# Kernel tuning notes

Measured on AMD Instinct MI355X. Metric: run time of the kernel, lower is better.

Reference implementation:

```python
import jax, jax.numpy as jnp
import numpy as np

D = 1024  # feature_size

def setup_inputs() -> dict:
    key = jax.random.key(0)
    ks = jax.random.split(key, 9)
    s = 1.0 / np.sqrt(D)
    inp = {"x": jax.random.normal(ks[0], (4, 2048, D), dtype=jnp.float32)}
    names = ["Wk", "Wq", "Wv", "Wo"]
    for i, n in enumerate(names):
        inp[n] = jax.random.uniform(ks[1 + 2 * i], (D, D), dtype=jnp.float32, minval=-s, maxval=s)
        inp["b" + n[1]] = jax.random.uniform(ks[2 + 2 * i], (D,), dtype=jnp.float32, minval=-s, maxval=s)
    return inp

def reference(x, Wk, bk, Wq, bq, Wv, bv, Wo, bo):
    # Linear layers: x @ W.T + b (torch nn.Linear convention)
    keys = jnp.einsum('bsd,ed->bse', x, Wk) + bk
    queries = jnp.einsum('bsd,ed->bse', x, Wq) + bq
    values = jnp.einsum('bsd,ed->bse', x, Wv) + bv
    scale = 1.0 / jnp.sqrt(jnp.float32(D))
    scores = jnp.einsum('bqd,bkd->bqk', queries, keys) * scale  # [B,S,S]
    attention = jax.nn.softmax(scores, axis=-1)
    out = jnp.einsum('bqk,bkd->bqd', attention, values)
    out = jnp.einsum('bsd,ed->bse', out, Wo) + bo
    return (out, attention)
```

## Files before the change

### kernel.cpp

```cpp
#include <hip/hip_runtime.h>
#include <hip/hip_bf16.h>


typedef __attribute__((ext_vector_type(8))) _Float16 f16x8;
typedef __attribute__((ext_vector_type(4))) _Float16 f16x4;
typedef __attribute__((ext_vector_type(4))) float f32x4;

static __device__ __forceinline__ void gl_lds16(const void* g, void* s) {
  __builtin_amdgcn_global_load_lds(
      (const __attribute__((address_space(1))) void*)g,
      (__attribute__((address_space(3))) void*)s, 16, 0, 0);
}

__global__ __launch_bounds__(256) void prep(
    const float* __restrict__ x,
    const float* __restrict__ Wq, const float* __restrict__ Wk,
    const float* __restrict__ Wo, const float* __restrict__ Wv,
    const float* __restrict__ bv, const float* __restrict__ bo,
    _Float16* __restrict__ xh, _Float16* __restrict__ Woh,
    _Float16* __restrict__ WvT, _Float16* __restrict__ WqT,
    _Float16* __restrict__ WkT, float* __restrict__ cpb) {
  const int b = blockIdx.x;
  const int tid = threadIdx.x;
  if (b < 8192) {
    const int i = b * 256 + tid;
    float4 v = reinterpret_cast<const float4*>(x)[i];
    f16x4 r = {(_Float16)v.x, (_Float16)v.y, (_Float16)v.z, (_Float16)v.w};
    reinterpret_cast<f16x4*>(xh)[i] = r;
  } else if (b < 9216) {
    const int i = (b - 8192) * 256 + tid;
    float4 v = reinterpret_cast<const float4*>(Wo)[i];
    f16x4 r = {(_Float16)v.x, (_Float16)v.y, (_Float16)v.z, (_Float16)v.w};
    reinterpret_cast<f16x4*>(Woh)[i] = r;
  } else if (b < 9984) {
    const int bb = b - 9216;
    const int which = bb >> 8;
    const float* src = which == 0 ? Wv : which == 1 ? Wq : Wk;
    _Float16* dst = which == 0 ? WvT : which == 1 ? WqT : WkT;
    __shared__ float t[64][65];
    const int tb = bb & 255;
    const int bx = (tb & 15) * 64, by = (tb >> 4) * 64;
    const int tx = tid & 63, ty = tid >> 6;
#pragma unroll
    for (int i = 0; i < 64; i += 4)
      t[ty + i][tx] = src[(long)(by + ty + i) * 1024 + bx + tx];
    __syncthreads();
#pragma unroll
    for (int i = 0; i < 64; i += 4)
      dst[(long)(bx + ty + i) * 1024 + by + tx] = (_Float16)t[tx][ty + i];
  } else {
    const int n = b - 9984;
    float s = 0.f;
    for (int d = tid; d < 1024; d += 256) s += Wo[(long)n * 1024 + d] * bv[d];
#pragma unroll
    for (int o = 32; o >= 1; o >>= 1) s += __shfl_xor(s, o);
    __shared__ float red[4];
    if ((tid & 63) == 0) red[tid >> 6] = s;
    __syncthreads();
    if (tid == 0) cpb[n] = red[0] + red[1] + red[2] + red[3] + bo[n];
  }
}

__global__ __launch_bounds__(256) void wkern(
    const float* __restrict__ bq, const float* __restrict__ bk,
    const _Float16* __restrict__ WkT, const _Float16* __restrict__ WqT,
    float* __restrict__ w1, float* __restrict__ w2, float* __restrict__ c0) {
  const int b = blockIdx.x;
  const int tid = threadIdx.x;
  float s = 0.f;
  if (b < 1024) {
    for (int e = tid; e < 1024; e += 256) s += bq[e] * (float)WkT[(long)b * 1024 + e];
  } else if (b < 2048) {
    const int d = b - 1024;
    for (int e = tid; e < 1024; e += 256) s += bk[e] * (float)WqT[(long)d * 1024 + e];
  } else {
    for (int e = tid; e < 1024; e += 256) s += bq[e] * bk[e];
  }
#pragma unroll
  for (int o = 32; o >= 1; o >>= 1) s += __shfl_xor(s, o);
  __shared__ float red[4];
  if ((tid & 63) == 0) red[tid >> 6] = s;
  __syncthreads();
  if (tid == 0) {
    const float v = red[0] + red[1] + red[2] + red[3];
    if (b < 1024) w1[b] = v;
    else if (b < 2048) w2[b - 1024] = v;
    else c0[0] = v;
  }
}

__global__ __launch_bounds__(256) void rowcol(
    const _Float16* __restrict__ xh, const float* __restrict__ w1,
    const float* __restrict__ w2, const float* __restrict__ c0,
    float* __restrict__ rowb, float* __restrict__ colb) {
  const long i = blockIdx.x;
  const int tid = threadIdx.x;
  f16x4 xv = reinterpret_cast<const f16x4*>(xh + i * 1024)[tid];
  float4 a1 = reinterpret_cast<const float4*>(w1)[tid];
  float4 a2 = reinterpret_cast<const float4*>(w2)[tid];
  float x0 = (float)xv[0], x1 = (float)xv[1], x2 = (float)xv[2], x3 = (float)xv[3];
  float d1 = x0 * a1.x + x1 * a1.y + x2 * a1.z + x3 * a1.w;
  float d2 = x0 * a2.x + x1 * a2.y + x2 * a2.z + x3 * a2.w;
#pragma unroll
  for (int o = 32; o >= 1; o >>= 1) { d1 += __shfl_xor(d1, o); d2 += __shfl_xor(d2, o); }
  __shared__ float r1[4], r2[4];
  if ((tid & 63) == 0) { r1[tid >> 6] = d1; r2[tid >> 6] = d2; }
  __syncthreads();
  if (tid == 0) {
    colb[i] = (r1[0] + r1[1] + r1[2] + r1[3]) * 0.03125f;
    rowb[i] = (r2[0] + r2[1] + r2[2] + r2[3] + c0[0]) * 0.03125f;
  }
}

template <int EPI, bool BB>
__global__ __launch_bounds__(256) void gemm128(
    const _Float16* __restrict__ A, const _Float16* __restrict__ B,
    const float* __restrict__ bias, float* __restrict__ Cf,
    _Float16* __restrict__ Ch, _Float16* __restrict__ C3,
    int M, int N, int K, long sA, long sB, long sC, float alpha, int panelW) {
  __shared__ _Float16 lds[3][2][4096];

  const unsigned gx = gridDim.x, gy = gridDim.y;
  const unsigned nwg = gx * gy * gridDim.z;
  unsigned flat = (blockIdx.z * gy + blockIdx.y) * gx + blockIdx.x;
  flat = (flat & 7) * (nwg >> 3) + (flat >> 3);
  const unsigned pb = gy * panelW;
  const long bz = flat / (gx * gy);
  const unsigned rem = flat % (gx * gy);
  const unsigned pi = rem / pb;
  const unsigned rem2 = rem % pb;
  const unsigned byi = rem2 / panelW;
  const unsigned bxi = pi * panelW + rem2 % panelW;

  const int tid = threadIdx.x;
  const int w = tid >> 6, lane = tid & 63;
  const int wr = w >> 1, wc = w & 1;
  const int lr = lane & 15, q = lane >> 4;
  const long row0 = (long)byi * 128;
  const long col0 = (long)bxi * 128;
  const int nt = K >> 5;

  const _Float16* pA = A + bz * sA;
  const _Float16* pB = BB ? (B + (row0 >> 11) * sB) : (B + bz * sB);

  f32x4 acc[4][4] = {};

  const int r0 = tid >> 2, c0i = ((tid & 3) - (r0 >> 1)) & 3;
  const int s1 = tid + 256;
  const int r1 = s1 >> 2, c1 = ((s1 & 3) - (r1 >> 1)) & 3;

  auto stage = [&](int kt) {
    if (kt >= nt) return;
    const int bf = kt % 3;
    const long gk = (long)kt * 32;
#pragma unroll
    for (int ab = 0; ab < 2; ++ab) {
      const _Float16* src = ab ? pB : pA;
      const long base = ab ? col0 : row0;
      gl_lds16(src + (base + r0) * (long)K + gk + c0i * 8, &lds[bf][ab][w << 9]);
      gl_lds16(src + (base + r1) * (long)K + gk + c1 * 8, &lds[bf][ab][2048 + (w << 9)]);
    }
  };
  auto rd = [&](int bf, int ab, int r) -> f16x8 {
    const int slot = (r << 2) + ((q + (r >> 1)) & 3);
    return *(const f16x8*)&lds[bf][ab][slot << 3];
  };

  stage(0); stage(1);
  asm volatile("s_waitcnt vmcnt(4)" ::: "memory");
  __builtin_amdgcn_s_barrier();
  __builtin_amdgcn_sched_barrier(0);

  for (int kt = 0; kt < nt; ++kt) {
    const int bf = kt % 3;
    stage(kt + 2);
    f16x8 a[4], b[4];
#pragma unroll
    for (int m = 0; m < 4; ++m) a[m] = rd(bf, 0, wr * 64 + m * 16 + lr);
#pragma unroll
    for (int n = 0; n < 4; ++n) b[n] = rd(bf, 1, wc * 64 + n * 16 + lr);
#pragma unroll
    for (int m = 0; m < 4; ++m)
#pragma unroll
      for (int n = 0; n < 4; ++n)
        acc[m][n] = __builtin_amdgcn_mfma_f32_16x16x32_f16(a[m], b[n], acc[m][n], 0, 0, 0);
    if (kt < nt - 2) asm volatile("s_waitcnt vmcnt(4)" ::: "memory");
    else             asm volatile("s_waitcnt vmcnt(0)" ::: "memory");
    __builtin_amdgcn_s_barrier();
    __builtin_amdgcn_sched_barrier(0);
  }

  if (EPI == 3 && col0 >= 1024) {
    _Float16* t = (_Float16*)&lds[0][0][0];
#pragma unroll
    for (int m = 0; m < 4; ++m)
#pragma unroll
      for (int n = 0; n < 4; ++n)
#pragma unroll
        for (int r = 0; r < 4; ++r) {
          const int rr = wr * 64 + m * 16 + q * 4 + r;
          const int cc = wc * 64 + n * 16 + lr;
          t[cc * 132 + rr] = (_Float16)(acc[m][n][r] * alpha);
        }
    __syncthreads();
    const long b2 = row0 >> 11;
    const long s2b = row0 & 2047;
    const int n = tid >> 1, s0 = (tid & 1) * 64;
    _Float16* dst = C3 + (b2 * 1024 + (col0 - 1024) + n) * 2048 + s2b + s0;
    const _Float16* srcT = t + n * 132 + s0;
#pragma unroll
    for (int j = 0; j < 8; ++j)
      *(f16x8*)(dst + j * 8) = *(const f16x8*)(srcT + j * 8);
    return;
  }

#pragma unroll
  for (int m = 0; m < 4; ++m)
#pragma unroll
    for (int n = 0; n < 4; ++n)
#pragma unroll
      for (int r = 0; r < 4; ++r) {
        const long row = row0 + wr * 64 + m * 16 + q * 4 + r;
        const long col = col0 + wc * 64 + n * 16 + lr;
        float v = acc[m][n][r] * alpha;
        if (EPI == 2) {
          v += Cf[bz * 2048 + row] + bias[bz * 2048 + col];
          Ch[bz * sC + row * (long)N + col] = (_Float16)v;
        } else if (EPI == 0) {
          if (bias) v += bias[col];
          Cf[bz * sC + row * (long)N + col] = v;
        } else if (EPI == 1) {
          if (bias) v += bias[col];
          Ch[bz * sC + row * (long)N + col] = (_Float16)v;
        } else {
          Ch[row * 1024 + col] = (_Float16)v;
        }
      }
}

__global__ __launch_bounds__(256) void softmax16(
    _Float16* __restrict__ Ph, float* __restrict__ attn) {
  const long row = blockIdx.x;
  _Float16* ph = Ph + row * 2048;
  float* ap = attn + row * 2048;
  const int tid = threadIdx.x;
  f16x8 v = reinterpret_cast<const f16x8*>(ph)[tid];
  float x[8];
#pragma unroll
  for (int j = 0; j < 8; ++j) x[j] = (float)v[j];
  float m = x[0];
#pragma unroll
  for (int j = 1; j < 8; ++j) m = fmaxf(m, x[j]);
#pragma unroll
  for (int o = 32; o >= 1; o >>= 1) m = fmaxf(m, __shfl_xor(m, o));
  __shared__ float red[4], red2[4];
  if ((tid & 63) == 0) red[tid >> 6] = m;
  __syncthreads();
  m = fmaxf(fmaxf(red[0], red[1]), fmaxf(red[2], red[3]));
  float s = 0.f;
#pragma unroll
  for (int j = 0; j < 8; ++j) { x[j] = expf(x[j] - m); s += x[j]; }
#pragma unroll
  for (int o = 32; o >= 1; o >>= 1) s += __shfl_xor(s, o);
  if ((tid & 63) == 0) red2[tid >> 6] = s;
  __syncthreads();
  s = red2[0] + red2[1] + red2[2] + red2[3];
  const float inv = 1.0f / s;
#pragma unroll
  for (int j = 0; j < 8; ++j) x[j] *= inv;
  reinterpret_cast<float4*>(ap)[tid * 2] = make_float4(x[0], x[1], x[2], x[3]);
  reinterpret_cast<float4*>(ap)[tid * 2 + 1] = make_float4(x[4], x[5], x[6], x[7]);
  f16x8 pv;
#pragma unroll
  for (int j = 0; j < 8; ++j) pv[j] = (_Float16)x[j];
  reinterpret_cast<f16x8*>(ph)[tid] = pv;
}

extern "C" void kernel_launch(void* const* d_in, const int* in_sizes, int n_in,
                              void* d_out, int out_size, void* d_ws, size_t ws_size,
                              hipStream_t stream) {
  const float* x  = (const float*)d_in[0];
  const float* Wk = (const float*)d_in[1];
  const float* bk = (const float*)d_in[2];
  const float* Wq = (const float*)d_in[3];
  const float* bq = (const float*)d_in[4];
  const float* Wv = (const float*)d_in[5];
  const float* bv = (const float*)d_in[6];
  const float* Wo = (const float*)d_in[7];
  const float* bo = (const float*)d_in[8];

  float* out  = (float*)d_out;
  float* attn = (float*)d_out + 8388608;

  const size_t MB = 1024 * 1024;
  unsigned char* ws = (unsigned char*)d_ws;
  _Float16* xh   = (_Float16*)(ws + 0 * MB);
  _Float16* Wf   = (_Float16*)(ws + 16 * MB);
  _Float16* WqT  = (_Float16*)(ws + 20 * MB);
  _Float16* Woh  = (_Float16*)(ws + 22 * MB);
  _Float16* WvT  = (_Float16*)(ws + 24 * MB);
  _Float16* WkT  = (_Float16*)(ws + 26 * MB);
  float*    rowb = (float*)   (ws + 28 * MB);
  float*    colb = (float*)   (ws + 28 * MB + 32768);
  float*    cpb  = (float*)   (ws + 28 * MB + 65536);
  float*    w1   = (float*)   (ws + 28 * MB + 69632);
  float*    w2   = (float*)   (ws + 28 * MB + 73728);
  float*    c0s  = (float*)   (ws + 28 * MB + 77824);
  _Float16* Y    = (_Float16*)(ws + 29 * MB);
  _Float16* Vt   = (_Float16*)(ws + 45 * MB);
  _Float16* Ph   = (_Float16*)(ws + 61 * MB);

  dim3 blk(256);
  const _Float16* nullh = nullptr;

  hipLaunchKernelGGL(prep, dim3(11008), blk, 0, stream,
                     x, Wq, Wk, Wo, Wv, bv, bo, xh, Woh, WvT, WqT, WkT, cpb);
  hipLaunchKernelGGL(wkern, dim3(2049), blk, 0, stream, bq, bk, WkT, WqT, w1, w2, c0s);
  hipLaunchKernelGGL((gemm128<1, false>), dim3(8, 8, 1), blk, 0, stream,
                     WkT, WqT, (const float*)nullptr, (float*)nullptr,
                     Wf, (_Float16*)nullh,
                     1024, 1024, 1024, 0L, 0L, 0L, 1.0f, 8);
  hipLaunchKernelGGL((gemm128<1, false>), dim3(8, 8, 1), blk, 0, stream,
                     Woh, WvT, (const float*)nullptr, (float*)nullptr,
                     Wf + 1048576, (_Float16*)nullh,
                     1024, 1024, 1024, 0L, 0L, 0L, 1.0f, 8);
  hipLaunchKernelGGL(rowcol, dim3(8192), blk, 0, stream, xh, w1, w2, c0s, rowb, colb);
  hipLaunchKernelGGL((gemm128<3, false>), dim3(16, 64, 1), blk, 0, stream,
                     xh, Wf, (const float*)nullptr, (float*)nullptr, Y, Vt,
                     8192, 2048, 1024, 0L, 0L, 0L, 1.0f, 8);
  hipLaunchKernelGGL((gemm128<2, false>), dim3(16, 16, 4), blk, 0, stream,
                     Y, xh, colb, rowb, Ph, (_Float16*)nullh,
                     2048, 2048, 1024, 2097152L, 2097152L, 4194304L, 0.03125f, 8);
  hipLaunchKernelGGL(softmax16, dim3(8192), blk, 0, stream, Ph, attn);
  hipLaunchKernelGGL((gemm128<0, true>), dim3(8, 64, 1), blk, 0, stream,
                     Ph, Vt, cpb, out, (_Float16*)nullh, (_Float16*)nullh,
                     8192, 1024, 2048, 0L, 2097152L, 0L, 1.0f, 4);
}
```

Before: 225.5 us.

## Add 256x256 eight-wave GEMM with phased ping-pong scheduling for projection and scores

Adds a new GEMM kernel with 256x256 tiles, 512 threads, a double-buffered LDS split into two K halves, and four phases per K-step. Each phase interleaves async global-to-LDS loads with MFMA bursts and raises wave priority around the math. It replaces the 128x128 kernel for the fused x@W projection (which also writes V transposed through a per-wave LDS staging buffer) and for the scores GEMM. The larger tiles raise data reuse per LDS byte and cut grid size. The cost is higher register pressure and fewer workgroups, which could hurt occupancy or tail balance.

```diff
diff --git a/kernel.cpp b/kernel.cpp
--- a/kernel.cpp
+++ b/kernel.cpp
@@ -112,11 +112,189 @@
   }
 }
 
+template <int EPI>
+__global__ __launch_bounds__(512, 2) void gemm256p8(
+    const _Float16* __restrict__ A, const _Float16* __restrict__ B,
+    const float* __restrict__ colb, const float* __restrict__ rowb,
+    _Float16* __restrict__ Ch, _Float16* __restrict__ C3,
+    int M, int N, int K, long sA, long sB, long sC, float alpha) {
+  __shared__ _Float16 lds[2][2][2][8192];
+
+  const unsigned gx = gridDim.x, gy = gridDim.y;
+  const unsigned nwg = gx * gy * gridDim.z;
+  unsigned flat = (blockIdx.z * gy + blockIdx.y) * gx + blockIdx.x;
+  flat = (flat & 7) * (nwg >> 3) + (flat >> 3);
+  const long bz = flat / (gx * gy);
+  const unsigned rem = flat % (gx * gy);
+  const unsigned byi = rem % gy;
+  const unsigned bxi = rem / gy;
+
+  const int tid = threadIdx.x;
+  const int w = tid >> 6, lane = tid & 63;
+  const int wr = w >> 2, wc = w & 3;
+  const int lr = lane & 15, q = lane >> 4;
+  const long row0 = (long)byi * 256;
+  const long col0 = (long)bxi * 256;
+  const int nt = K >> 6;
+
+  const _Float16* pA = A + bz * sA;
+  const _Float16* pB = B + bz * sB;
+
+  f32x4 acc[8][4] = {};
+
+  const int r0 = tid >> 2, c0i = ((tid & 3) - (r0 >> 1)) & 3;
+  const int s1 = tid + 512;
+  const int r1 = s1 >> 2, c1 = ((s1 & 3) - (r1 >> 1)) & 3;
+
+  auto stage = [&](int t, int ab, int kk) {
+    if (t >= nt) return;
+    const int d = t & 1;
+    const _Float16* src = ab ? pB : pA;
+    const long base = ab ? col0 : row0;
+    const long gk = (long)t * 64 + kk * 32;
+    gl_lds16(src + (base + r0) * (long)K + gk + c0i * 8, &lds[d][ab][kk][w << 9]);
+    gl_lds16(src + (base + r1) * (long)K + gk + c1 * 8,
+             &lds[d][ab][kk][4096 + (w << 9)]);
+  };
+  auto rd = [&](int d, int ab, int kk, int r) -> f16x8 {
+    const int slot = (r << 2) + ((q + (r >> 1)) & 3);
+    return *(const f16x8*)&lds[d][ab][kk][slot << 3];
+  };
+
+#define PH_SYNC()                                         \
+  __builtin_amdgcn_s_barrier();                           \
+  asm volatile("s_waitcnt lgkmcnt(0)" ::: "memory");      \
+  __builtin_amdgcn_sched_barrier(0);                      \
+  __builtin_amdgcn_s_setprio(1);
+#define PH_END()                                          \
+  __builtin_amdgcn_s_setprio(0);                          \
+  __builtin_amdgcn_sched_barrier(0);                      \
+  __builtin_amdgcn_s_barrier();
+
+  stage(0, 0, 0); stage(0, 1, 0); stage(0, 0, 1); stage(0, 1, 1);
+  stage(1, 1, 0); stage(1, 0, 0); stage(1, 1, 1);
+  asm volatile("s_waitcnt vmcnt(6)" ::: "memory");
+  __builtin_amdgcn_s_barrier();
+  __builtin_amdgcn_sched_barrier(0);
+
+  f16x8 a[4], b[4];
+  for (int t = 0; t < nt; ++t) {
+    const int d = t & 1;
+#pragma unroll
+    for (int mi = 0; mi < 4; ++mi) a[mi] = rd(d, 0, 0, wr * 128 + mi * 16 + lr);
+#pragma unroll
+    for (int n = 0; n < 4; ++n) b[n] = rd(d, 1, 0, wc * 64 + n * 16 + lr);
+    stage(t + 1, 0, 1);
+    PH_SYNC();
+#pragma unroll
+    for (int mi = 0; mi < 4; ++mi)
+#pragma unroll
+      for (int n = 0; n < 4; ++n)
+        acc[mi][n] = __builtin_amdgcn_mfma_f32_16x16x32_f16(a[mi], b[n], acc[mi][n], 0, 0, 0);
+    PH_END();
+#pragma unroll
+    for (int mi = 0; mi < 4; ++mi) a[mi] = rd(d, 0, 0, wr * 128 + 64 + mi * 16 + lr);
+    stage(t + 2, 1, 0);
+    PH_SYNC();
+#pragma unroll
+    for (int mi = 0; mi < 4; ++mi)
+#pragma unroll
+      for (int n = 0; n < 4; ++n)
+        acc[4 + mi][n] = __builtin_amdgcn_mfma_f32_16x16x32_f16(a[mi], b[n], acc[4 + mi][n], 0, 0, 0);
+    PH_END();
+#pragma unroll
+    for (int mi = 0; mi < 4; ++mi) a[mi] = rd(d, 0, 1, wr * 128 + mi * 16 + lr);
+#pragma unroll
+    for (int n = 0; n < 4; ++n) b[n] = rd(d, 1, 1, wc * 64 + n * 16 + lr);
+    stage(t + 2, 0, 0);
+    PH_SYNC();
+#pragma unroll
+    for (int mi = 0; mi < 4; ++mi)
+#pragma unroll
+      for (int n = 0; n < 4; ++n)
+        acc[mi][n] = __builtin_amdgcn_mfma_f32_16x16x32_f16(a[mi], b[n], acc[mi][n], 0, 0, 0);
+    PH_END();
+#pragma unroll
+    for (int mi = 0; mi < 4; ++mi) a[mi] = rd(d, 0, 1, wr * 128 + 64 + mi * 16 + lr);
+    stage(t + 2, 1, 1);
+    PH_SYNC();
+#pragma unroll
+    for (int mi = 0; mi < 4; ++mi)
+#pragma unroll
+      for (int n = 0; n < 4; ++n)
+        acc[4 + mi][n] = __builtin_amdgcn_mfma_f32_16x16x32_f16(a[mi], b[n], acc[4 + mi][n], 0, 0, 0);
+    __builtin_amdgcn_s_setprio(0);
+    __builtin_amdgcn_sched_barrier(0);
+    if (t + 2 < nt) asm volatile("s_waitcnt vmcnt(6)" ::: "memory");
+    else            asm volatile("s_waitcnt vmcnt(0)" ::: "memory");
+    __builtin_amdgcn_s_barrier();
+    __builtin_amdgcn_sched_barrier(0);
+  }
+#undef PH_SYNC
+#undef PH_END
+
+  if (EPI == 2) {
+#pragma unroll
+    for (int mi = 0; mi < 8; ++mi)
+#pragma unroll
+      for (int n = 0; n < 4; ++n)
+#pragma unroll
+        for (int r = 0; r < 4; ++r) {
+          const long row = row0 + wr * 128 + mi * 16 + q * 4 + r;
+          const long col = col0 + wc * 64 + n * 16 + lr;
+          float v = acc[mi][n][r] * alpha;
+          v += rowb[bz * 2048 + row] + colb[bz * 2048 + col];
+          Ch[bz * sC + row * (long)N + col] = (_Float16)v;
+        }
+  } else {
+    if (col0 < 1024) {
+#pragma unroll
+      for (int mi = 0; mi < 8; ++mi)
+#pragma unroll
+        for (int n = 0; n < 4; ++n)
+#pragma unroll
+          for (int r = 0; r < 4; ++r) {
+            const long row = row0 + wr * 128 + mi * 16 + q * 4 + r;
+            const long col = col0 + wc * 64 + n * 16 + lr;
+            Ch[row * 1024 + col] = (_Float16)(acc[mi][n][r] * alpha);
+          }
+    } else {
+      _Float16* wb = ((_Float16*)lds) + w * 4224;
+      const long b2 = row0 >> 11;
+      const long s2b = (row0 & 2047) + wr * 128;
+#pragma unroll
+      for (int ch = 0; ch < 2; ++ch) {
+#pragma unroll
+        for (int nn = 0; nn < 2; ++nn) {
+          const int n = ch * 2 + nn;
+#pragma unroll
+          for (int mi = 0; mi < 8; ++mi)
+#pragma unroll
+            for (int r = 0; r < 4; ++r) {
+              const int cl = nn * 16 + lr;
+              const int rl = mi * 16 + q * 4 + r;
+              wb[cl * 132 + rl] = (_Float16)(acc[mi][n][r] * alpha);
+            }
+        }
+        asm volatile("s_waitcnt lgkmcnt(0)" ::: "memory");
+        __builtin_amdgcn_sched_barrier(0);
+        const int cl = lane >> 1, sseg = (lane & 1) * 64;
+        _Float16* dst = C3 +
+            (b2 * 1024 + (col0 - 1024) + wc * 64 + ch * 32 + cl) * 2048 + s2b + sseg;
+        const _Float16* srcp = wb + cl * 132 + sseg;
+#pragma unroll
+        for (int j = 0; j < 8; ++j)
+          *(f16x8*)(dst + j * 8) = *(const f16x8*)(srcp + j * 8);
+      }
+    }
+  }
+}
+
 template <int EPI, bool BB>
 __global__ __launch_bounds__(256) void gemm128(
     const _Float16* __restrict__ A, const _Float16* __restrict__ B,
     const float* __restrict__ bias, float* __restrict__ Cf,
-    _Float16* __restrict__ Ch, _Float16* __restrict__ C3,
+    _Float16* __restrict__ Ch,
     int M, int N, int K, long sA, long sB, long sC, float alpha, int panelW) {
   __shared__ _Float16 lds[3][2][4096];
 
@@ -190,30 +368,6 @@
     __builtin_amdgcn_sched_barrier(0);
   }
 
-  if (EPI == 3 && col0 >= 1024) {
-    _Float16* t = (_Float16*)&lds[0][0][0];
-#pragma unroll
-    for (int m = 0; m < 4; ++m)
-#pragma unroll
-      for (int n = 0; n < 4; ++n)
-#pragma unroll
-        for (int r = 0; r < 4; ++r) {
-          const int rr = wr * 64 + m * 16 + q * 4 + r;
-          const int cc = wc * 64 + n * 16 + lr;
-          t[cc * 132 + rr] = (_Float16)(acc[m][n][r] * alpha);
-        }
-    __syncthreads();
-    const long b2 = row0 >> 11;
-    const long s2b = row0 & 2047;
-    const int n = tid >> 1, s0 = (tid & 1) * 64;
-    _Float16* dst = C3 + (b2 * 1024 + (col0 - 1024) + n) * 2048 + s2b + s0;
-    const _Float16* srcT = t + n * 132 + s0;
-#pragma unroll
-    for (int j = 0; j < 8; ++j)
-      *(f16x8*)(dst + j * 8) = *(const f16x8*)(srcT + j * 8);
-    return;
-  }
-
 #pragma unroll
   for (int m = 0; m < 4; ++m)
 #pragma unroll
@@ -223,18 +377,9 @@
         const long row = row0 + wr * 64 + m * 16 + q * 4 + r;
         const long col = col0 + wc * 64 + n * 16 + lr;
         float v = acc[m][n][r] * alpha;
-        if (EPI == 2) {
-          v += Cf[bz * 2048 + row] + bias[bz * 2048 + col];
-          Ch[bz * sC + row * (long)N + col] = (_Float16)v;
-        } else if (EPI == 0) {
-          if (bias) v += bias[col];
-          Cf[bz * sC + row * (long)N + col] = v;
-        } else if (EPI == 1) {
-          if (bias) v += bias[col];
-          Ch[bz * sC + row * (long)N + col] = (_Float16)v;
-        } else {
-          Ch[row * 1024 + col] = (_Float16)v;
-        }
+        if (bias) v += bias[col];
+        if (EPI == 0) Cf[bz * sC + row * (long)N + col] = v;
+        else          Ch[bz * sC + row * (long)N + col] = (_Float16)v;
       }
 }
 
@@ -311,28 +456,27 @@
   _Float16* Ph   = (_Float16*)(ws + 61 * MB);
 
   dim3 blk(256);
+  dim3 blk5(512);
   const _Float16* nullh = nullptr;
 
   hipLaunchKernelGGL(prep, dim3(11008), blk, 0, stream,
                      x, Wq, Wk, Wo, Wv, bv, bo, xh, Woh, WvT, WqT, WkT, cpb);
   hipLaunchKernelGGL(wkern, dim3(2049), blk, 0, stream, bq, bk, WkT, WqT, w1, w2, c0s);
   hipLaunchKernelGGL((gemm128<1, false>), dim3(8, 8, 1), blk, 0, stream,
-                     WkT, WqT, (const float*)nullptr, (float*)nullptr,
-                     Wf, (_Float16*)nullh,
+                     WkT, WqT, (const float*)nullptr, (float*)nullptr, Wf,
                      1024, 1024, 1024, 0L, 0L, 0L, 1.0f, 8);
   hipLaunchKernelGGL((gemm128<1, false>), dim3(8, 8, 1), blk, 0, stream,
                      Woh, WvT, (const float*)nullptr, (float*)nullptr,
-                     Wf + 1048576, (_Float16*)nullh,
-                     1024, 1024, 1024, 0L, 0L, 0L, 1.0f, 8);
+                     Wf + 1048576, 1024, 1024, 1024, 0L, 0L, 0L, 1.0f, 8);
   hipLaunchKernelGGL(rowcol, dim3(8192), blk, 0, stream, xh, w1, w2, c0s, rowb, colb);
-  hipLaunchKernelGGL((gemm128<3, false>), dim3(16, 64, 1), blk, 0, stream,
-                     xh, Wf, (const float*)nullptr, (float*)nullptr, Y, Vt,
-                     8192, 2048, 1024, 0L, 0L, 0L, 1.0f, 8);
-  hipLaunchKernelGGL((gemm128<2, false>), dim3(16, 16, 4), blk, 0, stream,
+  hipLaunchKernelGGL((gemm256p8<3>), dim3(8, 32, 1), blk5, 0, stream,
+                     xh, Wf, (const float*)nullptr, (const float*)nullptr, Y, Vt,
+                     8192, 2048, 1024, 0L, 0L, 0L, 1.0f);
+  hipLaunchKernelGGL((gemm256p8<2>), dim3(8, 8, 4), blk5, 0, stream,
                      Y, xh, colb, rowb, Ph, (_Float16*)nullh,
-                     2048, 2048, 1024, 2097152L, 2097152L, 4194304L, 0.03125f, 8);
+                     2048, 2048, 1024, 2097152L, 2097152L, 4194304L, 0.03125f);
   hipLaunchKernelGGL(softmax16, dim3(8192), blk, 0, stream, Ph, attn);
   hipLaunchKernelGGL((gemm128<0, true>), dim3(8, 64, 1), blk, 0, stream,
-                     Ph, Vt, cpb, out, (_Float16*)nullh, (_Float16*)nullh,
+                     Ph, Vt, cpb, out, (_Float16*)nullh,
                      8192, 1024, 2048, 0L, 2097152L, 0L, 1.0f, 4);
 }
```

After: 216.3 us. -4.1%, faster.
